# Performance work log

Measured on AMD Instinct MI355X. Metric: run time of the kernel, lower is better.

## Reference

```python
import jax, jax.numpy as jnp
import numpy as np

B, L, H, V = 16, 512, 256, 32000
HALF = H // 2
EPS_LN = 1e-5
EPS_NORM = 1e-12


def setup_inputs() -> dict:
    key = jax.random.key(0)
    ks = jax.random.split(key, 9)
    s = 0.02
    return {
        "seq": jax.random.randint(ks[0], (B, L), 0, V),
        "embed": jax.random.normal(ks[1], (V, H), jnp.float32) * s,
        "W1": jax.random.normal(ks[2], (2 * H, H), jnp.float32) * s,
        "b1": jnp.zeros((2 * H,), jnp.float32),
        "W2": jax.random.normal(ks[3], (H, 2 * H), jnp.float32) * s,
        "b2": jnp.zeros((H,), jnp.float32),
        "gamma": jnp.ones((H,), jnp.float32),
        "beta": jnp.zeros((H,), jnp.float32),
        "W_sem": jax.random.normal(ks[4], (HALF, H), jnp.float32) * s,
        "W_epi": jax.random.normal(ks[5], (HALF, H), jnp.float32) * s,
        "W_rp": jax.random.normal(ks[6], (H, H), jnp.float32) * s,
        "b_rp": jnp.zeros((H,), jnp.float32),
        "W_out": jax.random.normal(ks[7], (V, H), jnp.float32) * s,
        "b_out": jnp.zeros((V,), jnp.float32),
    }


def _l2norm(x):
    # F.normalize(dim=-1): x / max(||x||, eps)
    n = jnp.sqrt(jnp.sum(x * x, axis=-1, keepdims=True))
    return x / jnp.maximum(n, EPS_NORM)


def reference(seq, embed, W1, b1, W2, b2, gamma, beta, W_sem, W_epi, W_rp, b_rp, W_out, b_out):
    h = embed[seq]                                   # [B, L, H]
    ff = jnp.maximum(h @ W1.T + b1, 0.0) @ W2.T + b2  # MLP with 2H hidden
    x = h + ff
    mu = jnp.mean(x, axis=-1, keepdims=True)
    var = jnp.var(x, axis=-1, keepdims=True)
    h = (x - mu) / jnp.sqrt(var + EPS_LN) * gamma + beta  # LayerNorm

    ks_all = jnp.einsum('blh,kh->blk', h, W_sem)     # [B, L, HALF]
    ke_all = jnp.einsum('blh,kh->blk', h, W_epi)

    def step(carry, kv):
        M_s, M_e = carry
        k_s, k_e = kv                                 # [B, HALF] each
        kns = _l2norm(k_s)
        kne = _l2norm(k_e)
        vps = jnp.einsum('bij,bj->bi', M_s, kns)      # read from fast weights
        vpe = jnp.einsum('bij,bj->bi', M_e, kne)
        M_s = M_s + jnp.einsum('bi,bj->bij', k_s - vps, kns)  # delta-rule write
        M_e = M_e + jnp.einsum('bi,bj->bij', k_e - vpe, kne)
        return (M_s, M_e), None

    M0 = jnp.zeros((B, HALF, HALF), h.dtype)
    # scan over timesteps 0..L-2 (time-major)
    (M_s, M_e), _ = jax.lax.scan(
        step, (M0, M0),
        (jnp.swapaxes(ks_all[:, :-1], 0, 1), jnp.swapaxes(ke_all[:, :-1], 0, 1)))

    cs = jnp.einsum('bij,bj->bi', M_s, ks_all[:, -1])  # read with last-token query
    ce = jnp.einsum('bij,bj->bi', M_e, ke_all[:, -1])
    c = jnp.concatenate([cs, ce], axis=-1)             # [B, H]
    r = c @ W_rp.T + b_rp
    return r @ W_out.T + b_out                          # [B, V]
```

## Files before the change

### kernel.cpp

```cpp
#include <hip/hip_runtime.h>

#define B_ 16
#define L_ 512
#define H_ 256
#define V_ 32000
#define HALF_ 128

typedef __attribute__((ext_vector_type(8))) short short8;
typedef __attribute__((ext_vector_type(4))) float floatx4;

__device__ __forceinline__ unsigned short f2bf(float x) {
  unsigned int u = __float_as_uint(x);
  unsigned int r = (u + 0x7FFFu + ((u >> 16) & 1u)) >> 16;
  return (unsigned short)r;
}

template <int CTRL>
__device__ __forceinline__ float dpp_xor_add(float x) {
  int y = __builtin_amdgcn_mov_dpp(__float_as_int(x), CTRL, 0xf, 0xf, true);
  return x + __int_as_float(y);
}

__device__ __forceinline__ float redu16(float p) {
  p = dpp_xor_add<0xB1>(p);
  p = dpp_xor_add<0x4E>(p);
  p = dpp_xor_add<0x141>(p);
  p = dpp_xor_add<0x140>(p);
  return p;
}

__device__ __forceinline__ void async_cp16(const float* g, float* l) {
  __builtin_amdgcn_global_load_lds(
      (const __attribute__((address_space(1))) void*)g,
      (__attribute__((address_space(3))) void*)l, 16, 0, 0);
}

__global__ __launch_bounds__(256) void prep_kernel(const int* __restrict__ seq,
                                                   const float* __restrict__ embed,
                                                   float* __restrict__ h,
                                                   unsigned short* __restrict__ hbf,
                                                   const float* __restrict__ W1,
                                                   const float* __restrict__ W2,
                                                   const float* __restrict__ Ws,
                                                   const float* __restrict__ We,
                                                   unsigned short* __restrict__ W1b,
                                                   unsigned short* __restrict__ W2b,
                                                   unsigned short* __restrict__ Wcb) {
  int blk = blockIdx.x;
  int tid = threadIdx.x;
  if (blk < 2048) {
    int token = blk * 4 + (tid >> 6);
    int lane = tid & 63;
    int row = seq[token];
    float4 v = ((const float4*)(embed + (size_t)row * H_))[lane];
    ((float4*)(h + (size_t)token * H_))[lane] = v;
    ushort4 o;
    o.x = f2bf(v.x); o.y = f2bf(v.y); o.z = f2bf(v.z); o.w = f2bf(v.w);
    *(ushort4*)(hbf + (size_t)token * H_ + lane * 4) = o;
  } else {
    int i = (blk - 2048) * 256 + tid;
    if (i < 131072) W1b[i] = f2bf(W1[i]);
    else if (i < 262144) W2b[i - 131072] = f2bf(W2[i - 131072]);
    else if (i < 294912) Wcb[i - 262144] = f2bf(Ws[i - 262144]);
    else Wcb[i - 262144] = f2bf(We[i - 294912]);
  }
}

template <int MT, bool RELU, bool BIAS, bool RES, bool OUT_BF16>
__global__ __launch_bounds__(256) void gemm_mfma(const unsigned short* __restrict__ A,
                                                 const unsigned short* __restrict__ Bw,
                                                 const float* __restrict__ bias,
                                                 const float* __restrict__ Res,
                                                 float* __restrict__ Cf,
                                                 unsigned short* __restrict__ Cb,
                                                 int M, int N, int K) {
  constexpr int FI = MT / 32;
  __shared__ unsigned short As[MT * 40];
  __shared__ unsigned short Bs[128 * 40];
  int tid = threadIdx.x;
  int wave = tid >> 6, lane = tid & 63;
  int wm = (wave >> 1) * (MT / 2), wn = (wave & 1) * 64;
  int quad = lane >> 4, l15 = lane & 15;
  int bm = blockIdx.y * MT, bn = blockIdx.x * 128;
  int sr = tid >> 2, sq = tid & 3;

  floatx4 zero = {0.f, 0.f, 0.f, 0.f};
  floatx4 acc[FI][4];
#pragma unroll
  for (int fi = 0; fi < FI; fi++)
#pragma unroll
    for (int fj = 0; fj < 4; fj++) acc[fi][fj] = zero;

  uint4 av0, av1, bv0, bv1;
  av0 = *(const uint4*)(A + (size_t)(bm + sr) * K + sq * 8);
  if (MT == 128) av1 = *(const uint4*)(A + (size_t)(bm + 64 + sr) * K + sq * 8);
  bv0 = *(const uint4*)(Bw + (size_t)(bn + sr) * K + sq * 8);
  bv1 = *(const uint4*)(Bw + (size_t)(bn + 64 + sr) * K + sq * 8);

  for (int k0 = 0; k0 < K; k0 += 32) {
    __syncthreads();
    *(uint4*)(As + sr * 40 + sq * 8) = av0;
    if (MT == 128) *(uint4*)(As + (64 + sr) * 40 + sq * 8) = av1;
    *(uint4*)(Bs + sr * 40 + sq * 8) = bv0;
    *(uint4*)(Bs + (64 + sr) * 40 + sq * 8) = bv1;
    __syncthreads();
    if (k0 + 32 < K) {
      av0 = *(const uint4*)(A + (size_t)(bm + sr) * K + k0 + 32 + sq * 8);
      if (MT == 128) av1 = *(const uint4*)(A + (size_t)(bm + 64 + sr) * K + k0 + 32 + sq * 8);
      bv0 = *(const uint4*)(Bw + (size_t)(bn + sr) * K + k0 + 32 + sq * 8);
      bv1 = *(const uint4*)(Bw + (size_t)(bn + 64 + sr) * K + k0 + 32 + sq * 8);
    }
    short8 af[FI], bf[4];
#pragma unroll
    for (int f = 0; f < FI; f++) af[f] = *(const short8*)(As + (wm + f * 16 + l15) * 40 + quad * 8);
#pragma unroll
    for (int f = 0; f < 4; f++) bf[f] = *(const short8*)(Bs + (wn + f * 16 + l15) * 40 + quad * 8);
#pragma unroll
    for (int fi = 0; fi < FI; fi++)
#pragma unroll
      for (int fj = 0; fj < 4; fj++)
        acc[fi][fj] = __builtin_amdgcn_mfma_f32_16x16x32_bf16(af[fi], bf[fj], acc[fi][fj], 0, 0, 0);
  }

#pragma unroll
  for (int fi = 0; fi < FI; fi++) {
#pragma unroll
    for (int fj = 0; fj < 4; fj++) {
      int col = bn + wn + fj * 16 + l15;
      float bb = BIAS ? bias[col] : 0.f;
#pragma unroll
      for (int rg = 0; rg < 4; rg++) {
        int row = bm + wm + fi * 16 + quad * 4 + rg;
        float v = acc[fi][fj][rg] + bb;
        if (RES) v += Res[(size_t)row * N + col];
        if (RELU) v = fmaxf(v, 0.f);
        if (OUT_BF16) Cb[(size_t)row * N + col] = f2bf(v);
        else Cf[(size_t)row * N + col] = v;
      }
    }
  }
}

__global__ __launch_bounds__(256) void kproj_kernel(const float* __restrict__ hx,
                                                    const float* __restrict__ gma,
                                                    const float* __restrict__ bta,
                                                    const unsigned short* __restrict__ Wcb,
                                                    float* __restrict__ khat,
                                                    float* __restrict__ kT) {
  __shared__ unsigned short As[32 * 40];
  __shared__ unsigned short Bs[256 * 40];
  __shared__ float mus[32], ivs[32];
  int tid = threadIdx.x;
  int wave = tid >> 6, lane = tid & 63;
  int wm = (wave >> 1) * 16, wnh = wave & 1, wn = wnh * 128;
  int quad = lane >> 4, l15 = lane & 15;
  int bm = blockIdx.x * 32;

  {
    int row = tid >> 3, jj = tid & 7;
    const float4* hr = (const float4*)(hx + (size_t)(bm + row) * H_ + jj * 32);
    float s = 0.f, sq = 0.f;
#pragma unroll
    for (int q = 0; q < 8; q++) {
      float4 v = hr[q];
      s += (v.x + v.y) + (v.z + v.w);
      sq += (v.x * v.x + v.y * v.y) + (v.z * v.z + v.w * v.w);
    }
    s = dpp_xor_add<0xB1>(s);  sq = dpp_xor_add<0xB1>(sq);
    s = dpp_xor_add<0x4E>(s);  sq = dpp_xor_add<0x4E>(sq);
    s = dpp_xor_add<0x141>(s); sq = dpp_xor_add<0x141>(sq);
    float mu = s * (1.f / H_);
    float var = sq * (1.f / H_) - mu * mu;
    if (jj == 0) { mus[row] = mu; ivs[row] = rsqrtf(var + 1e-5f); }
  }

  floatx4 zero = {0.f, 0.f, 0.f, 0.f};
  floatx4 acc[8];
#pragma unroll
  for (int fj = 0; fj < 8; fj++) acc[fj] = zero;

  int sr = tid >> 2, sq4 = tid & 3;
  float4 af0, af1, gf0, gf1, bt0, bt1;
  uint4 bv[4];
  if (tid < 128) {
    const float4* ap = (const float4*)(hx + (size_t)(bm + sr) * H_ + sq4 * 8);
    af0 = ap[0]; af1 = ap[1];
    const float4* gp = (const float4*)(gma + sq4 * 8); gf0 = gp[0]; gf1 = gp[1];
    const float4* bp = (const float4*)(bta + sq4 * 8); bt0 = bp[0]; bt1 = bp[1];
  }
#pragma unroll
  for (int q = 0; q < 4; q++) {
    int unit = q * 256 + tid;
    bv[q] = *(const uint4*)(Wcb + (size_t)(unit >> 2) * H_ + (unit & 3) * 8);
  }

  for (int k0 = 0; k0 < 256; k0 += 32) {
    __syncthreads();
    if (tid < 128) {
      float mu = mus[sr], iv = ivs[sr];
      ushort4 lo, hi;
      lo.x = f2bf((af0.x - mu) * iv * gf0.x + bt0.x);
      lo.y = f2bf((af0.y - mu) * iv * gf0.y + bt0.y);
      lo.z = f2bf((af0.z - mu) * iv * gf0.z + bt0.z);
      lo.w = f2bf((af0.w - mu) * iv * gf0.w + bt0.w);
      hi.x = f2bf((af1.x - mu) * iv * gf1.x + bt1.x);
      hi.y = f2bf((af1.y - mu) * iv * gf1.y + bt1.y);
      hi.z = f2bf((af1.z - mu) * iv * gf1.z + bt1.z);
      hi.w = f2bf((af1.w - mu) * iv * gf1.w + bt1.w);
      *(ushort4*)(As + sr * 40 + sq4 * 8) = lo;
      *(ushort4*)(As + sr * 40 + sq4 * 8 + 4) = hi;
    }
#pragma unroll
    for (int q = 0; q < 4; q++) {
      int unit = q * 256 + tid;
      *(uint4*)(Bs + (unit >> 2) * 40 + (unit & 3) * 8) = bv[q];
    }
    __syncthreads();
    if (k0 + 32 < 256) {
      if (tid < 128) {
        const float4* ap = (const float4*)(hx + (size_t)(bm + sr) * H_ + k0 + 32 + sq4 * 8);
        af0 = ap[0]; af1 = ap[1];
        const float4* gp = (const float4*)(gma + k0 + 32 + sq4 * 8); gf0 = gp[0]; gf1 = gp[1];
        const float4* bp = (const float4*)(bta + k0 + 32 + sq4 * 8); bt0 = bp[0]; bt1 = bp[1];
      }
#pragma unroll
      for (int q = 0; q < 4; q++) {
        int unit = q * 256 + tid;
        bv[q] = *(const uint4*)(Wcb + (size_t)(unit >> 2) * H_ + k0 + 32 + (unit & 3) * 8);
      }
    }
    short8 af = *(const short8*)(As + (wm + l15) * 40 + quad * 8);
    short8 bf[8];
#pragma unroll
    for (int fj = 0; fj < 8; fj++)
      bf[fj] = *(const short8*)(Bs + (wn + fj * 16 + l15) * 40 + quad * 8);
#pragma unroll
    for (int fj = 0; fj < 8; fj++)
      acc[fj] = __builtin_amdgcn_mfma_f32_16x16x32_bf16(af, bf[fj], acc[fj], 0, 0, 0);
  }

  int b = bm >> 9;
  int idxm = b * 2 + wnh;
  int tloc0 = (bm & 511) + wm + quad * 4;
  float inv[4];
#pragma unroll
  for (int rg = 0; rg < 4; rg++) {
    float ssq = 0.f;
#pragma unroll
    for (int fj = 0; fj < 8; fj++) ssq += acc[fj][rg] * acc[fj][rg];
    ssq = redu16(ssq);
    inv[rg] = 1.f / fmaxf(sqrtf(ssq), 1e-12f);
  }
#pragma unroll
  for (int fj = 0; fj < 8; fj++) {
    int ch = fj * 16 + l15;
    int j = ch >> 2, e = ch & 3;
    int pj = (j & 1) ? (16 + (j >> 1)) : (j >> 1);
    int pcol = pj * 4 + e;
#pragma unroll
    for (int rg = 0; rg < 4; rg++)
      khat[((size_t)idxm * L_ + tloc0 + rg) * HALF_ + pcol] = acc[fj][rg] * inv[rg];
    float4 raw = {acc[fj][0], acc[fj][1], acc[fj][2], acc[fj][3]};
    *(float4*)(kT + (size_t)idxm * (HALF_ * L_) + (size_t)ch * L_ + tloc0) = raw;
  }
}

#define STEP(KP, KR)                                                     \
  do {                                                                   \
    float t0_ = m[0] * KP[0] + m[1] * KP[1];                             \
    float t1_ = m[2] * KP[2] + m[3] * KP[3];                             \
    float t2_ = m[4] * KP[4] + m[5] * KP[5];                             \
    float t3_ = m[6] * KP[6] + m[7] * KP[7];                             \
    float p_ = (t0_ + t1_) + (t2_ + t3_);                                \
    p_ = redu16(p_);                                                     \
    float s_ = (KR) - p_;                                                \
    m[0] += s_ * KP[0]; m[1] += s_ * KP[1]; m[2] += s_ * KP[2];          \
    m[3] += s_ * KP[3]; m[4] += s_ * KP[4]; m[5] += s_ * KP[5];          \
    m[6] += s_ * KP[6]; m[7] += s_ * KP[7];                              \
  } while (0)

__global__ __launch_bounds__(256) void scan_kernel(const float* __restrict__ khat,
                                                   const float* __restrict__ kT,
                                                   float* __restrict__ c) {
  __shared__ float sk[2][64 * 128];
  int bid = blockIdx.x;
  int idxm = bid & 31;
  int rg = bid >> 5;
  int b = idxm >> 1, mat = idxm & 1;
  const float* kh = khat + (size_t)idxm * L_ * HALF_;
  const float* kTi = kT + (size_t)idxm * HALF_ * L_;

  int tid = threadIdx.x;
  int wave = tid >> 6, lane = tid & 63;
  int seg = tid & 15, rl = tid >> 4;
  int r = rg * 16 + rl;
  int c0 = seg * 8;
  const float* krow = kTi + (size_t)r * L_;

  float m[8];
#pragma unroll
  for (int g = 0; g < 8; g++) m[g] = 0.f;

  {
    const float* g0 = kh + wave * 2048 + lane * 4;
    float* l0 = &sk[0][wave * 2048];
#pragma unroll
    for (int j = 0; j < 8; j++) async_cp16(g0 + j * 256, l0 + j * 256);
  }
  __syncthreads();

  float4 krn = *(const float4*)(krow);
  const float* lb = &sk[0][0] + seg * 4;

  for (int ch = 0; ch < 7; ch++) {
    {
      const float* gs = kh + (size_t)(ch + 1) * 8192 + wave * 2048 + lane * 4;
      float* ls = &sk[(ch + 1) & 1][wave * 2048];
#pragma unroll
      for (int j = 0; j < 8; j++) async_cp16(gs + j * 256, ls + j * 256);
    }
    const float* base = lb + (ch & 1) * 8192;
    float pk[4][8];
#pragma unroll
    for (int u = 0; u < 4; u++) {
      *(float4*)&pk[u][0] = *(const float4*)(base + u * 128);
      *(float4*)&pk[u][4] = *(const float4*)(base + u * 128 + 64);
    }
    for (int g = 0; g < 15; g++) {
      float4 krc = krn;
      krn = *(const float4*)(krow + ch * 64 + g * 4 + 4);
#pragma unroll
      for (int u = 0; u < 4; u++) {
        STEP(pk[u], ((u == 0) ? krc.x : (u == 1) ? krc.y : (u == 2) ? krc.z : krc.w));
        int tn = g * 4 + u + 4;
        *(float4*)&pk[u][0] = *(const float4*)(base + tn * 128);
        *(float4*)&pk[u][4] = *(const float4*)(base + tn * 128 + 64);
      }
    }
    {
      float4 krc = krn;
      krn = *(const float4*)(krow + ch * 64 + 64);
      STEP(pk[0], krc.x);
      STEP(pk[1], krc.y);
      STEP(pk[2], krc.z);
      STEP(pk[3], krc.w);
    }
    __syncthreads();
  }

  {
    const float* base = lb + 8192;
    float pk[4][8];
#pragma unroll
    for (int u = 0; u < 4; u++) {
      *(float4*)&pk[u][0] = *(const float4*)(base + u * 128);
      *(float4*)&pk[u][4] = *(const float4*)(base + u * 128 + 64);
    }
    for (int g = 0; g < 15; g++) {
      float4 krc = krn;
      krn = *(const float4*)(krow + 448 + g * 4 + 4);
#pragma unroll
      for (int u = 0; u < 4; u++) {
        STEP(pk[u], ((u == 0) ? krc.x : (u == 1) ? krc.y : (u == 2) ? krc.z : krc.w));
        int tn = g * 4 + u + 4;
        *(float4*)&pk[u][0] = *(const float4*)(base + tn * 128);
        *(float4*)&pk[u][4] = *(const float4*)(base + tn * 128 + 64);
      }
    }
    float4 krc = krn;
    STEP(pk[0], krc.x);
    STEP(pk[1], krc.y);
    STEP(pk[2], krc.z);
  }

  float q[8];
#pragma unroll
  for (int j = 0; j < 8; j++) q[j] = kTi[(size_t)(c0 + j) * L_ + 511];
  float t0 = m[0] * q[0] + m[1] * q[1];
  float t1 = m[2] * q[2] + m[3] * q[3];
  float t2 = m[4] * q[4] + m[5] * q[5];
  float t3 = m[6] * q[6] + m[7] * q[7];
  float p = redu16((t0 + t1) + (t2 + t3));
  if (seg == 0) c[(size_t)b * H_ + mat * HALF_ + r] = p;
}

__global__ void rp_kernel(const float* __restrict__ c, const float* __restrict__ Wrp,
                          const float* __restrict__ brp, float* __restrict__ r) {
  int b = blockIdx.x;
  int n = threadIdx.x;
  __shared__ float cs[H_];
  cs[n] = c[(size_t)b * H_ + n];
  __syncthreads();
  const float4* w4 = (const float4*)(Wrp + (size_t)n * H_);
  const float4* c4 = (const float4*)cs;
  float acc = 0.f;
#pragma unroll 8
  for (int k = 0; k < H_ / 4; k++) {
    float4 w = w4[k], cc = c4[k];
    acc += w.x * cc.x + w.y * cc.y + w.z * cc.z + w.w * cc.w;
  }
  r[(size_t)b * H_ + n] = acc + brp[n];
}

__global__ __launch_bounds__(256) void out_kernel(const float* __restrict__ r,
                                                  const float* __restrict__ Wout,
                                                  const float* __restrict__ bout,
                                                  float* __restrict__ out) {
  __shared__ float rs[16 * 272];
  __shared__ float obuf[16 * 68];
  int tid = threadIdx.x;
#pragma unroll
  for (int q = 0; q < 16; q++) {
    int idx = q * 256 + tid;
    int bb = idx >> 8, cc = idx & 255;
    rs[bb * 272 + cc + 4 * (cc >> 6)] = r[idx];
  }
  __syncthreads();
  int row = tid >> 2, part = tid & 3;
  int v = blockIdx.x * 64 + row;
  const float4* w4 = (const float4*)(Wout + (size_t)v * H_ + part * 64);
  float acc[16];
#pragma unroll
  for (int bb = 0; bb < 16; bb++) acc[bb] = 0.f;
#pragma unroll 4
  for (int j = 0; j < 16; j++) {
    float4 w = w4[j];
#pragma unroll
    for (int bb = 0; bb < 16; bb++) {
      float4 rv = *(const float4*)&rs[bb * 272 + part * 68 + j * 4];
      acc[bb] += w.x * rv.x + w.y * rv.y + w.z * rv.z + w.w * rv.w;
    }
  }
  float bo = bout[v];
#pragma unroll
  for (int bb = 0; bb < 16; bb++) {
    acc[bb] = dpp_xor_add<0xB1>(acc[bb]);
    acc[bb] = dpp_xor_add<0x4E>(acc[bb]);
  }
#pragma unroll
  for (int q = 0; q < 4; q++) {
    int bb = part * 4 + q;
    obuf[bb * 68 + row] = acc[bb] + bo;
  }
  __syncthreads();
#pragma unroll
  for (int q = 0; q < 4; q++) {
    int idx = q * 256 + tid;
    int bb = idx >> 6, vl = idx & 63;
    out[(size_t)bb * V_ + blockIdx.x * 64 + vl] = obuf[bb * 68 + vl];
  }
}

extern "C" void kernel_launch(void* const* d_in, const int* in_sizes, int n_in,
                              void* d_out, int out_size, void* d_ws, size_t ws_size,
                              hipStream_t stream) {
  const int* seq = (const int*)d_in[0];
  const float* embed = (const float*)d_in[1];
  const float* W1 = (const float*)d_in[2];
  const float* b1 = (const float*)d_in[3];
  const float* W2 = (const float*)d_in[4];
  const float* b2 = (const float*)d_in[5];
  const float* gamma = (const float*)d_in[6];
  const float* beta = (const float*)d_in[7];
  const float* Wsem = (const float*)d_in[8];
  const float* Wepi = (const float*)d_in[9];
  const float* Wrp = (const float*)d_in[10];
  const float* brp = (const float*)d_in[11];
  const float* Wout = (const float*)d_in[12];
  const float* bout = (const float*)d_in[13];
  float* out = (float*)d_out;

  float* ws = (float*)d_ws;
  float* h = ws;
  unsigned short* a1b = (unsigned short*)(ws + 2097152);
  float* khat = ws + 2097152;
  unsigned short* hbf = (unsigned short*)(ws + 4194304);
  float* kT = ws + 4194304;
  unsigned short* W1b = (unsigned short*)(ws + 6291456);
  unsigned short* W2b = (unsigned short*)(ws + 6356992);
  unsigned short* Wcb = (unsigned short*)(ws + 6422528);
  float* c = ws + 6455296;
  float* r = ws + 6459392;

  prep_kernel<<<3328, 256, 0, stream>>>(seq, embed, h, hbf, W1, W2, Wsem, Wepi, W1b, W2b, Wcb);
  gemm_mfma<128, true, true, false, true><<<dim3(4, 64), 256, 0, stream>>>(
      hbf, W1b, b1, nullptr, nullptr, a1b, 8192, 512, 256);
  gemm_mfma<64, false, true, true, false><<<dim3(2, 128), 256, 0, stream>>>(
      a1b, W2b, b2, h, h, nullptr, 8192, 256, 512);
  kproj_kernel<<<256, 256, 0, stream>>>(h, gamma, beta, Wcb, khat, kT);
  scan_kernel<<<256, 256, 0, stream>>>(khat, kT, c);
  rp_kernel<<<16, 256, 0, stream>>>(c, Wrp, brp, r);
  out_kernel<<<500, 256, 0, stream>>>(r, Wout, bout, out);
}
```

Before: 222.9 us.

## Break delta-rule scan dependency using precomputed key Gram dot products

Adds a gram_kernel that precomputes the dot products of each normalized key with the previous one and two back. The scan then finds each step's read value from a stale M·k plus corrections built from those Gram terms, so the cross-lane reduction no longer sits on the serial critical path. This is meant to cut per-step latency in the sequential recurrence. In exchange it adds a kernel launch, more registers (an 8-slot key buffer), and a different floating-point summation order.

After: 228.0 us. 1.02x slower.

```diff
diff --git a/kernel.cpp b/kernel.cpp
--- a/kernel.cpp
+++ b/kernel.cpp
@@ -33,6 +33,11 @@
   __builtin_amdgcn_global_load_lds(
       (const __attribute__((address_space(1))) void*)g,
       (__attribute__((address_space(3))) void*)l, 16, 0, 0);
+}
+
+__device__ __forceinline__ float dot8t(const float* a, const float* b) {
+  return ((a[0] * b[0] + a[1] * b[1]) + (a[2] * b[2] + a[3] * b[3])) +
+         ((a[4] * b[4] + a[5] * b[5]) + (a[6] * b[6] + a[7] * b[7]));
 }
 
 __global__ __launch_bounds__(256) void prep_kernel(const int* __restrict__ seq,
@@ -265,24 +270,100 @@
   }
 }
 
-#define STEP(KP, KR)                                                     \
-  do {                                                                   \
-    float t0_ = m[0] * KP[0] + m[1] * KP[1];                             \
-    float t1_ = m[2] * KP[2] + m[3] * KP[3];                             \
-    float t2_ = m[4] * KP[4] + m[5] * KP[5];                             \
-    float t3_ = m[6] * KP[6] + m[7] * KP[7];                             \
-    float p_ = (t0_ + t1_) + (t2_ + t3_);                                \
-    p_ = redu16(p_);                                                     \
-    float s_ = (KR) - p_;                                                \
-    m[0] += s_ * KP[0]; m[1] += s_ * KP[1]; m[2] += s_ * KP[2];          \
-    m[3] += s_ * KP[3]; m[4] += s_ * KP[4]; m[5] += s_ * KP[5];          \
-    m[6] += s_ * KP[6]; m[7] += s_ * KP[7];                              \
+__global__ __launch_bounds__(256) void gram_kernel(const float* __restrict__ khat,
+                                                   float* __restrict__ G) {
+  int bid = blockIdx.x;
+  int im = bid & 31, part = bid >> 5;
+  int tid = threadIdx.x;
+  int seg = tid & 15, rl = tid >> 4;
+  const float* kh = khat + (size_t)im * L_ * HALF_ + seg * 8;
+  float* g1 = G + im * 1024;
+  float* g2 = g1 + 512;
+#pragma unroll
+  for (int tb = 0; tb < 4; tb++) {
+    int t = part * 64 + tb * 16 + rl;
+    float a[8], b1[8], b2[8];
+    *(float4*)&a[0] = *(const float4*)(kh + (size_t)t * HALF_);
+    *(float4*)&a[4] = *(const float4*)(kh + (size_t)t * HALF_ + 4);
+    float d1 = 0.f, d2 = 0.f;
+    if (t >= 1) {
+      *(float4*)&b1[0] = *(const float4*)(kh + (size_t)(t - 1) * HALF_);
+      *(float4*)&b1[4] = *(const float4*)(kh + (size_t)(t - 1) * HALF_ + 4);
+      d1 = redu16(dot8t(a, b1));
+    }
+    if (t >= 2) {
+      *(float4*)&b2[0] = *(const float4*)(kh + (size_t)(t - 2) * HALF_);
+      *(float4*)&b2[4] = *(const float4*)(kh + (size_t)(t - 2) * HALF_ + 4);
+      d2 = redu16(dot8t(a, b2));
+    }
+    if (seg == 0) { g1[t] = d1; g2[t] = d2; }
+  }
+}
+
+
+#define UPD8(SL)                                                          \
+  do {                                                                    \
+    m[0] += sp1 * pk[SL][0]; m[1] += sp1 * pk[SL][1];                     \
+    m[2] += sp1 * pk[SL][2]; m[3] += sp1 * pk[SL][3];                     \
+    m[4] += sp1 * pk[SL][4]; m[5] += sp1 * pk[SL][5];                     \
+    m[6] += sp1 * pk[SL][6]; m[7] += sp1 * pk[SL][7];                     \
+  } while (0)
+
+#define PSTEP(SU, SD, KR, G1V, G2V)                                       \
+  do {                                                                    \
+    UPD8(SU);                                                             \
+    float dn_ = redu16(dot8t(m, pk[SD]));                                 \
+    float p_ = (pD0 + sp2 * (G2V)) + sp1 * (G1V);                         \
+    float s_ = (KR) - p_;                                                 \
+    sp2 = sp1; sp1 = s_; pD0 = pD1; pD1 = dn_;                            \
+  } while (0)
+
+#define PSTEP_NODN(SU, KR, G1V, G2V)                                      \
+  do {                                                                    \
+    UPD8(SU);                                                             \
+    float p_ = (pD0 + sp2 * (G2V)) + sp1 * (G1V);                         \
+    float s_ = (KR) - p_;                                                 \
+    sp2 = sp1; sp1 = s_; pD0 = pD1;                                       \
+  } while (0)
+
+#define LOADSLOT(S, LT)                                                   \
+  do {                                                                    \
+    *(float4*)&pk[S][0] = *(const float4*)(bufbase + (LT) * 128);         \
+    *(float4*)&pk[S][4] = *(const float4*)(bufbase + (LT) * 128 + 64);    \
+  } while (0)
+
+#define ITER8(LT, T, DO47)                                                \
+  do {                                                                    \
+    LOADSLOT(4, (LT) + 4);                                                \
+    krB = *(const float4*)(krow + (T) + 4);                               \
+    g1B = *(const float4*)&gg[(T) + 4];                                   \
+    g2B = *(const float4*)&gg[512 + (T) + 4];                             \
+    PSTEP(7, 2, krA.x, g1A.x, g2A.x);                                     \
+    LOADSLOT(5, (LT) + 5);                                                \
+    PSTEP(0, 3, krA.y, g1A.y, g2A.y);                                     \
+    LOADSLOT(6, (LT) + 6);                                                \
+    PSTEP(1, 4, krA.z, g1A.z, g2A.z);                                     \
+    LOADSLOT(7, (LT) + 7);                                                \
+    PSTEP(2, 5, krA.w, g1A.w, g2A.w);                                     \
+    if (DO47) LOADSLOT(0, (LT) + 8);                                      \
+    krA = *(const float4*)(krow + (T) + 8);                               \
+    g1A = *(const float4*)&gg[(T) + 8];                                   \
+    g2A = *(const float4*)&gg[512 + (T) + 8];                             \
+    PSTEP(3, 6, krB.x, g1B.x, g2B.x);                                     \
+    if (DO47) LOADSLOT(1, (LT) + 9);                                      \
+    PSTEP(4, 7, krB.y, g1B.y, g2B.y);                                     \
+    if (DO47) LOADSLOT(2, (LT) + 10);                                     \
+    PSTEP(5, 0, krB.z, g1B.z, g2B.z);                                     \
+    if (DO47) LOADSLOT(3, (LT) + 11);                                     \
+    PSTEP(6, 1, krB.w, g1B.w, g2B.w);                                     \
   } while (0)
 
 __global__ __launch_bounds__(256) void scan_kernel(const float* __restrict__ khat,
                                                    const float* __restrict__ kT,
+                                                   const float* __restrict__ G,
                                                    float* __restrict__ c) {
   __shared__ float sk[2][64 * 128];
+  __shared__ float gg[1024];
   int bid = blockIdx.x;
   int idxm = bid & 31;
   int rg = bid >> 5;
@@ -306,81 +387,65 @@
     float* l0 = &sk[0][wave * 2048];
 #pragma unroll
     for (int j = 0; j < 8; j++) async_cp16(g0 + j * 256, l0 + j * 256);
+    *(float4*)(gg + tid * 4) = *(const float4*)(G + idxm * 1024 + tid * 4);
   }
   __syncthreads();
 
-  float4 krn = *(const float4*)(krow);
   const float* lb = &sk[0][0] + seg * 4;
-
-  for (int ch = 0; ch < 7; ch++) {
-    {
+  const float* bufbase = lb;
+  float pk[8][8];
+  float pD0 = 0.f, pD1 = 0.f, sp1 = 0.f, sp2 = 0.f;
+  float4 krA, krB, g1A, g1B, g2A, g2B;
+  krA = *(const float4*)(krow);
+  g1A = *(const float4*)&gg[0];
+  g2A = *(const float4*)&gg[512];
+  LOADSLOT(0, 0); LOADSLOT(1, 1); LOADSLOT(2, 2); LOADSLOT(3, 3);
+
+  for (int ch = 0; ch < 8; ch++) {
+    bufbase = lb + (ch & 1) * 8192;
+    if (ch < 7) {
       const float* gs = kh + (size_t)(ch + 1) * 8192 + wave * 2048 + lane * 4;
       float* ls = &sk[(ch + 1) & 1][wave * 2048];
 #pragma unroll
       for (int j = 0; j < 8; j++) async_cp16(gs + j * 256, ls + j * 256);
     }
-    const float* base = lb + (ch & 1) * 8192;
-    float pk[4][8];
-#pragma unroll
-    for (int u = 0; u < 4; u++) {
-      *(float4*)&pk[u][0] = *(const float4*)(base + u * 128);
-      *(float4*)&pk[u][4] = *(const float4*)(base + u * 128 + 64);
-    }
-    for (int g = 0; g < 15; g++) {
-      float4 krc = krn;
-      krn = *(const float4*)(krow + ch * 64 + g * 4 + 4);
-#pragma unroll
-      for (int u = 0; u < 4; u++) {
-        STEP(pk[u], ((u == 0) ? krc.x : (u == 1) ? krc.y : (u == 2) ? krc.z : krc.w));
-        int tn = g * 4 + u + 4;
-        *(float4*)&pk[u][0] = *(const float4*)(base + tn * 128);
-        *(float4*)&pk[u][4] = *(const float4*)(base + tn * 128 + 64);
-      }
-    }
-    {
-      float4 krc = krn;
-      krn = *(const float4*)(krow + ch * 64 + 64);
-      STEP(pk[0], krc.x);
-      STEP(pk[1], krc.y);
-      STEP(pk[2], krc.z);
-      STEP(pk[3], krc.w);
+    if (ch > 0) {
+      UPD8(7);
+      LOADSLOT(0, 0); LOADSLOT(1, 1); LOADSLOT(2, 2); LOADSLOT(3, 3);
+      pD0 = redu16(dot8t(m, pk[0]));
+      pD1 = redu16(dot8t(m, pk[1]));
+      sp1 = 0.f; sp2 = 0.f;
+    }
+    int T0 = ch * 64;
+    for (int it = 0; it < 7; ++it) {
+      int lt = it * 8;
+      ITER8(lt, T0 + lt, 1);
+    }
+    if (ch < 7) {
+      ITER8(56, T0 + 56, 0);
+    } else {
+      LOADSLOT(4, 60);
+      krB = *(const float4*)(krow + 508);
+      g1B = *(const float4*)&gg[508];
+      g2B = *(const float4*)&gg[512 + 508];
+      PSTEP(7, 2, krA.x, g1A.x, g2A.x);
+      LOADSLOT(5, 61);
+      PSTEP(0, 3, krA.y, g1A.y, g2A.y);
+      LOADSLOT(6, 62);
+      PSTEP(1, 4, krA.z, g1A.z, g2A.z);
+      PSTEP(2, 5, krA.w, g1A.w, g2A.w);
+      PSTEP(3, 6, krB.x, g1B.x, g2B.x);
+      PSTEP_NODN(4, krB.y, g1B.y, g2B.y);
+      PSTEP_NODN(5, krB.z, g1B.z, g2B.z);
+      UPD8(6);
     }
     __syncthreads();
   }
 
-  {
-    const float* base = lb + 8192;
-    float pk[4][8];
-#pragma unroll
-    for (int u = 0; u < 4; u++) {
-      *(float4*)&pk[u][0] = *(const float4*)(base + u * 128);
-      *(float4*)&pk[u][4] = *(const float4*)(base + u * 128 + 64);
-    }
-    for (int g = 0; g < 15; g++) {
-      float4 krc = krn;
-      krn = *(const float4*)(krow + 448 + g * 4 + 4);
-#pragma unroll
-      for (int u = 0; u < 4; u++) {
-        STEP(pk[u], ((u == 0) ? krc.x : (u == 1) ? krc.y : (u == 2) ? krc.z : krc.w));
-        int tn = g * 4 + u + 4;
-        *(float4*)&pk[u][0] = *(const float4*)(base + tn * 128);
-        *(float4*)&pk[u][4] = *(const float4*)(base + tn * 128 + 64);
-      }
-    }
-    float4 krc = krn;
-    STEP(pk[0], krc.x);
-    STEP(pk[1], krc.y);
-    STEP(pk[2], krc.z);
-  }
-
   float q[8];
 #pragma unroll
   for (int j = 0; j < 8; j++) q[j] = kTi[(size_t)(c0 + j) * L_ + 511];
-  float t0 = m[0] * q[0] + m[1] * q[1];
-  float t1 = m[2] * q[2] + m[3] * q[3];
-  float t2 = m[4] * q[4] + m[5] * q[5];
-  float t3 = m[6] * q[6] + m[7] * q[7];
-  float p = redu16((t0 + t1) + (t2 + t3));
+  float p = redu16(dot8t(m, q));
   if (seg == 0) c[(size_t)b * H_ + mat * HALF_ + r] = p;
 }
 
@@ -481,6 +546,7 @@
   unsigned short* Wcb = (unsigned short*)(ws + 6422528);
   float* c = ws + 6455296;
   float* r = ws + 6459392;
+  float* G = ws + 6463488;
 
   prep_kernel<<<3328, 256, 0, stream>>>(seq, embed, h, hbf, W1, W2, Wsem, Wepi, W1b, W2b, Wcb);
   gemm_mfma<128, true, true, false, true><<<dim3(4, 64), 256, 0, stream>>>(
@@ -488,7 +554,8 @@
   gemm_mfma<64, false, true, true, false><<<dim3(2, 128), 256, 0, stream>>>(
       a1b, W2b, b2, h, h, nullptr, 8192, 256, 512);
   kproj_kernel<<<256, 256, 0, stream>>>(h, gamma, beta, Wcb, khat, kT);
-  scan_kernel<<<256, 256, 0, stream>>>(khat, kT, c);
+  gram_kernel<<<256, 256, 0, stream>>>(khat, G);
+  scan_kernel<<<256, 256, 0, stream>>>(khat, kT, G, c);
   rp_kernel<<<16, 256, 0, stream>>>(c, Wrp, brp, r);
   out_kernel<<<500, 256, 0, stream>>>(r, Wout, bout, out);
 }
```

## Split scan rows across 32 lanes with 4 columns each, doubling scan blocks

Applied to the files above, without the earlier changes.

The delta-rule scan now gives each matrix row to 32 lanes holding 4 columns apiece instead of 16 lanes holding 8, so each block covers 8 rows and the grid doubles to 512 blocks. The reduction gains an extra ds_swizzle step across 32 lanes, and the LDS read index uses the permuted column layout written by kproj. The intent is to shorten the serial per-step dependency chain of FMAs and to raise occupancy. The cost is a longer cross-lane reduction per timestep, and each block reloads the full khat tile, doubling global and LDS traffic for the same work.

Measured after the change: 233.5 us. +4.8%, slower.

```diff
diff --git a/kernel.cpp b/kernel.cpp
--- a/kernel.cpp
+++ b/kernel.cpp
@@ -27,6 +27,12 @@
   p = dpp_xor_add<0x141>(p);
   p = dpp_xor_add<0x140>(p);
   return p;
+}
+
+__device__ __forceinline__ float redu32(float p) {
+  p = redu16(p);
+  int y = __builtin_amdgcn_ds_swizzle(__float_as_int(p), 0x401F);
+  return p + __int_as_float(y);
 }
 
 __device__ __forceinline__ void async_cp16(const float* g, float* l) {
@@ -265,18 +271,14 @@
   }
 }
 
-#define STEP(KP, KR)                                                     \
-  do {                                                                   \
-    float t0_ = m[0] * KP[0] + m[1] * KP[1];                             \
-    float t1_ = m[2] * KP[2] + m[3] * KP[3];                             \
-    float t2_ = m[4] * KP[4] + m[5] * KP[5];                             \
-    float t3_ = m[6] * KP[6] + m[7] * KP[7];                             \
-    float p_ = (t0_ + t1_) + (t2_ + t3_);                                \
-    p_ = redu16(p_);                                                     \
-    float s_ = (KR) - p_;                                                \
-    m[0] += s_ * KP[0]; m[1] += s_ * KP[1]; m[2] += s_ * KP[2];          \
-    m[3] += s_ * KP[3]; m[4] += s_ * KP[4]; m[5] += s_ * KP[5];          \
-    m[6] += s_ * KP[6]; m[7] += s_ * KP[7];                              \
+
+#define STEP32(PK, KR)                                               \
+  do {                                                               \
+    float p_ = (m0 * PK.x + m1 * PK.y) + (m2 * PK.z + m3 * PK.w);    \
+    p_ = redu32(p_);                                                 \
+    float s_ = (KR) - p_;                                            \
+    m0 += s_ * PK.x; m1 += s_ * PK.y;                                \
+    m2 += s_ * PK.z; m3 += s_ * PK.w;                                \
   } while (0)
 
 __global__ __launch_bounds__(256) void scan_kernel(const float* __restrict__ khat,
@@ -292,14 +294,14 @@
 
   int tid = threadIdx.x;
   int wave = tid >> 6, lane = tid & 63;
-  int seg = tid & 15, rl = tid >> 4;
-  int r = rg * 16 + rl;
-  int c0 = seg * 8;
+  int rl = tid >> 5;
+  int l32 = tid & 31;
+  int r = rg * 8 + rl;
+  int pj = (l32 & 1) ? (16 + (l32 >> 1)) : (l32 >> 1);
+  int c0 = l32 * 4;
   const float* krow = kTi + (size_t)r * L_;
 
-  float m[8];
-#pragma unroll
-  for (int g = 0; g < 8; g++) m[g] = 0.f;
+  float m0 = 0.f, m1 = 0.f, m2 = 0.f, m3 = 0.f;
 
   {
     const float* g0 = kh + wave * 2048 + lane * 4;
@@ -310,7 +312,7 @@
   __syncthreads();
 
   float4 krn = *(const float4*)(krow);
-  const float* lb = &sk[0][0] + seg * 4;
+  const float* lb = &sk[0][0] + pj * 4;
 
   for (int ch = 0; ch < 7; ch++) {
     {
@@ -320,68 +322,55 @@
       for (int j = 0; j < 8; j++) async_cp16(gs + j * 256, ls + j * 256);
     }
     const float* base = lb + (ch & 1) * 8192;
-    float pk[4][8];
-#pragma unroll
-    for (int u = 0; u < 4; u++) {
-      *(float4*)&pk[u][0] = *(const float4*)(base + u * 128);
-      *(float4*)&pk[u][4] = *(const float4*)(base + u * 128 + 64);
-    }
+    float4 pk0 = *(const float4*)(base + 0 * 128);
+    float4 pk1 = *(const float4*)(base + 1 * 128);
+    float4 pk2 = *(const float4*)(base + 2 * 128);
+    float4 pk3 = *(const float4*)(base + 3 * 128);
     for (int g = 0; g < 15; g++) {
       float4 krc = krn;
       krn = *(const float4*)(krow + ch * 64 + g * 4 + 4);
-#pragma unroll
-      for (int u = 0; u < 4; u++) {
-        STEP(pk[u], ((u == 0) ? krc.x : (u == 1) ? krc.y : (u == 2) ? krc.z : krc.w));
-        int tn = g * 4 + u + 4;
-        *(float4*)&pk[u][0] = *(const float4*)(base + tn * 128);
-        *(float4*)&pk[u][4] = *(const float4*)(base + tn * 128 + 64);
-      }
+      STEP32(pk0, krc.x); pk0 = *(const float4*)(base + (g * 4 + 4) * 128);
+      STEP32(pk1, krc.y); pk1 = *(const float4*)(base + (g * 4 + 5) * 128);
+      STEP32(pk2, krc.z); pk2 = *(const float4*)(base + (g * 4 + 6) * 128);
+      STEP32(pk3, krc.w); pk3 = *(const float4*)(base + (g * 4 + 7) * 128);
     }
     {
       float4 krc = krn;
       krn = *(const float4*)(krow + ch * 64 + 64);
-      STEP(pk[0], krc.x);
-      STEP(pk[1], krc.y);
-      STEP(pk[2], krc.z);
-      STEP(pk[3], krc.w);
+      STEP32(pk0, krc.x);
+      STEP32(pk1, krc.y);
+      STEP32(pk2, krc.z);
+      STEP32(pk3, krc.w);
     }
     __syncthreads();
   }
 
   {
     const float* base = lb + 8192;
-    float pk[4][8];
-#pragma unroll
-    for (int u = 0; u < 4; u++) {
-      *(float4*)&pk[u][0] = *(const float4*)(base + u * 128);
-      *(float4*)&pk[u][4] = *(const float4*)(base + u * 128 + 64);
-    }
+    float4 pk0 = *(const float4*)(base + 0 * 128);
+    float4 pk1 = *(const float4*)(base + 1 * 128);
+    float4 pk2 = *(const float4*)(base + 2 * 128);
+    float4 pk3 = *(const float4*)(base + 3 * 128);
     for (int g = 0; g < 15; g++) {
       float4 krc = krn;
       krn = *(const float4*)(krow + 448 + g * 4 + 4);
-#pragma unroll
-      for (int u = 0; u < 4; u++) {
-        STEP(pk[u], ((u == 0) ? krc.x : (u == 1) ? krc.y : (u == 2) ? krc.z : krc.w));
-        int tn = g * 4 + u + 4;
-        *(float4*)&pk[u][0] = *(const float4*)(base + tn * 128);
-        *(float4*)&pk[u][4] = *(const float4*)(base + tn * 128 + 64);
-      }
+      STEP32(pk0, krc.x); pk0 = *(const float4*)(base + (g * 4 + 4) * 128);
+      STEP32(pk1, krc.y); pk1 = *(const float4*)(base + (g * 4 + 5) * 128);
+      STEP32(pk2, krc.z); pk2 = *(const float4*)(base + (g * 4 + 6) * 128);
+      STEP32(pk3, krc.w); pk3 = *(const float4*)(base + (g * 4 + 7) * 128);
     }
     float4 krc = krn;
-    STEP(pk[0], krc.x);
-    STEP(pk[1], krc.y);
-    STEP(pk[2], krc.z);
-  }
-
-  float q[8];
-#pragma unroll
-  for (int j = 0; j < 8; j++) q[j] = kTi[(size_t)(c0 + j) * L_ + 511];
-  float t0 = m[0] * q[0] + m[1] * q[1];
-  float t1 = m[2] * q[2] + m[3] * q[3];
-  float t2 = m[4] * q[4] + m[5] * q[5];
-  float t3 = m[6] * q[6] + m[7] * q[7];
-  float p = redu16((t0 + t1) + (t2 + t3));
-  if (seg == 0) c[(size_t)b * H_ + mat * HALF_ + r] = p;
+    STEP32(pk0, krc.x);
+    STEP32(pk1, krc.y);
+    STEP32(pk2, krc.z);
+  }
+
+  float q0 = kTi[(size_t)(c0 + 0) * L_ + 511];
+  float q1 = kTi[(size_t)(c0 + 1) * L_ + 511];
+  float q2 = kTi[(size_t)(c0 + 2) * L_ + 511];
+  float q3 = kTi[(size_t)(c0 + 3) * L_ + 511];
+  float p = redu32((m0 * q0 + m1 * q1) + (m2 * q2 + m3 * q3));
+  if (l32 == 0) c[(size_t)b * H_ + mat * HALF_ + r] = p;
 }
 
 __global__ void rp_kernel(const float* __restrict__ c, const float* __restrict__ Wrp,
@@ -488,7 +477,7 @@
   gemm_mfma<64, false, true, true, false><<<dim3(2, 128), 256, 0, stream>>>(
       a1b, W2b, b2, h, h, nullptr, 8192, 256, 512);
   kproj_kernel<<<256, 256, 0, stream>>>(h, gamma, beta, Wcb, khat, kT);
-  scan_kernel<<<256, 256, 0, stream>>>(khat, kT, c);
+  scan_kernel<<<512, 256, 0, stream>>>(khat, kT, c);
   rp_kernel<<<16, 256, 0, stream>>>(c, Wrp, brp, r);
   out_kernel<<<500, 256, 0, stream>>>(r, Wout, bout, out);
 }
```
